# Kernel tuning notes

Measured on AMD Instinct MI355X. Metric: run time of the kernel, lower is better.

## Reference

```python
import jax, jax.numpy as jnp
import numpy as np

D = 128          # embed_dim
NSYM = 100000    # num_symbols
PAD = NSYM       # padding idx (zero row)
B = 2048         # query batch
FEW = 5          # support set size
M = 128          # max neighbors
KTAB = 64        # knn table width
K = 32           # knn_k topk
STEPS = 4        # process_steps
DM = 2 * D       # d_model for encoders (256)
HID = 2 * DM     # LSTM hidden (512)


def _cos(a, b):
    # torch F.cosine_similarity, eps=1e-8; a [B,1,d], b [B,N,d] -> [B,N]
    num = jnp.sum(a * b, axis=-1)
    den = jnp.maximum(jnp.linalg.norm(a, axis=-1) * jnp.linalg.norm(b, axis=-1), 1e-8)
    return num / den


def _l2n(x):
    return x / jnp.maximum(jnp.linalg.norm(x, axis=-1, keepdims=True), 1e-12)


def _neighbor_encoder(conn, ids, knn_tab, emb, gcn_w, gcn_w_b, gcn_b, gate_w, gate_b):
    rel = emb[conn[..., 0]]                      # [N,M,D]
    ent = emb[conn[..., 1]]                      # [N,M,D]
    center = emb[ids][:, None, :]                # [N,1,D]
    sim = _cos(center, ent)                      # [N,M]
    _, idx = jax.lax.top_k(sim, K)               # [N,K]
    rel_k = jnp.take_along_axis(rel, idx[..., None], axis=1)
    ent_k = jnp.take_along_axis(ent, idx[..., None], axis=1)
    h = jnp.concatenate([rel_k, ent_k], axis=-1) @ gcn_w.T + gcn_w_b + gcn_b
    struct = jnp.tanh(h.mean(axis=1))            # [N,D]
    # knn branch: gather knn neighbor ids, cosine topk, pad-relation embeds (zero row)
    kent = emb[knn_tab[ids]]                     # [N,KTAB,D]
    sim2 = _cos(center, kent)
    _, idx2 = jax.lax.top_k(sim2, K)
    kent_k = jnp.take_along_axis(kent, idx2[..., None], axis=1)
    pad_row = jax.lax.stop_gradient(emb[PAD])    # padding_idx row (zeros, no grad)
    krel = jnp.broadcast_to(pad_row, kent_k.shape)
    h2 = jnp.concatenate([krel, kent_k], axis=-1) @ gcn_w.T + gcn_w_b + gcn_b
    knn_mean = jnp.tanh(h2.mean(axis=1))         # [N,D]
    alpha = jax.nn.sigmoid(jnp.concatenate([struct, knn_mean], axis=-1) @ gate_w.T + gate_b)
    return (1.0 - alpha) * struct + alpha * knn_mean


def _support_encoder(x, p1_w, p1_b, p2_w, p2_b, ln_g, ln_b):
    o = jax.nn.relu(x @ p1_w.T + p1_b) @ p2_w.T + p2_b
    z = o + x
    mu = z.mean(axis=-1, keepdims=True)
    sig = z.std(axis=-1, ddof=1, keepdims=True)  # torch unbiased std
    return (z - mu) / (sig + 1e-3) * ln_g + ln_b


def _query_encoder(support, query, w_ih, w_hh, b_ih, b_hh):
    # attLSTM processing block; support [1,DM], query [B,DM]
    n = query.shape[0]
    h_r = jnp.zeros((n, HID), query.dtype)
    c = jnp.zeros((n, HID), query.dtype)
    h = query
    for _ in range(STEPS):
        g = query @ w_ih.T + b_ih + h_r @ w_hh.T + b_hh
        i, f, gg, o = jnp.split(g, 4, axis=-1)
        c = jax.nn.sigmoid(f) * c + jax.nn.sigmoid(i) * jnp.tanh(gg)
        h_ = jax.nn.sigmoid(o) * jnp.tanh(c)
        h = query + h_[:, :DM]
        attn = jax.nn.softmax(h @ support.T, axis=1)  # [B,1]
        r = attn @ support                             # [B,DM]
        h_r = jnp.concatenate([h, r], axis=1)
    return h


def _forward(query, support, q_l_conn, q_r_conn, s_l_conn, s_r_conn, knn_neighbors,
             emb, gcn_w, gcn_w_b, gcn_b, gate_w, gate_b,
             p1_w, p1_b, p2_w, p2_b, ln_g, ln_b, w_ih, w_hh, b_ih, b_hh):
    ne = lambda conn, ids: _neighbor_encoder(conn, ids, knn_neighbors, emb,
                                             gcn_w, gcn_w_b, gcn_b, gate_w, gate_b)
    ql = ne(q_l_conn, query[:, 0])
    qr = ne(q_r_conn, query[:, 1])
    sl = ne(s_l_conn, support[:, 0])
    sr = ne(s_r_conn, support[:, 1])
    qn = jnp.concatenate([ql, qr], axis=-1)   # [B,DM]
    sn = jnp.concatenate([sl, sr], axis=-1)   # [FEW,DM]
    se = lambda x: _support_encoder(x, p1_w, p1_b, p2_w, p2_b, ln_g, ln_b)
    support_g = se(sn).mean(axis=0, keepdims=True)  # [1,DM]
    query_g = se(qn)                                 # [B,DM]
    query_f = _l2n(_query_encoder(support_g, query_g, w_ih, w_hh, b_ih, b_hh))
    sg = _l2n(support_g[0])
    return query_f @ sg                              # [B]


def setup_inputs() -> dict:
    key = jax.random.key(0)
    ks = jax.random.split(key, 24)
    f = lambda i, shape, s=0.05: jax.random.normal(ks[i], shape, dtype=jnp.float32) * s
    ri = lambda i, shape: jax.random.randint(ks[i], shape, 0, NSYM).astype(jnp.int32)
    emb = f(0, (NSYM + 1, D), 0.5).at[PAD].set(0.0)
    return dict(
        query=ri(1, (B, 2)), support=ri(2, (FEW, 2)),
        q_l_conn=ri(3, (B, M, 2)),
        q_l_deg=jax.random.randint(ks[4], (B,), 1, M).astype(jnp.int32),
        q_r_conn=ri(5, (B, M, 2)),
        q_r_deg=jax.random.randint(ks[6], (B,), 1, M).astype(jnp.int32),
        s_l_conn=ri(7, (FEW, M, 2)),
        s_l_deg=jax.random.randint(ks[8], (FEW,), 1, M).astype(jnp.int32),
        s_r_conn=ri(9, (FEW, M, 2)),
        s_r_deg=jax.random.randint(ks[10], (FEW,), 1, M).astype(jnp.int32),
        knn_neighbors=ri(11, (NSYM + 1, KTAB)),
        emb=emb,
        gcn_w=f(12, (D, 2 * D)), gcn_w_b=f(13, (D,)),
        gcn_b=jnp.zeros((D,), jnp.float32),
        gate_w=f(14, (1, 2 * D)), gate_b=jnp.zeros((1,), jnp.float32),
        p1_w=f(15, (2 * DM, DM)), p1_b=f(16, (2 * DM,)),
        p2_w=f(17, (DM, 2 * DM)), p2_b=f(18, (DM,)),
        ln_g=jnp.ones((DM,), jnp.float32), ln_b=jnp.zeros((DM,), jnp.float32),
        w_ih=f(19, (4 * HID, DM)), w_hh=f(20, (4 * HID, HID)),
        b_ih=f(21, (4 * HID,)), b_hh=f(22, (4 * HID,)),
    )


def reference(query, support, q_l_conn, q_l_deg, q_r_conn, q_r_deg,
              s_l_conn, s_l_deg, s_r_conn, s_r_deg, knn_neighbors,
              emb, gcn_w, gcn_w_b, gcn_b, gate_w, gate_b,
              p1_w, p1_b, p2_w, p2_b, ln_g, ln_b, w_ih, w_hh, b_ih, b_hh):
    # degrees are computed-but-unused in this fork's neighbor_encoder (plain mean)
    return _forward(query, support, q_l_conn, q_r_conn, s_l_conn, s_r_conn, knn_neighbors,
                    emb, gcn_w, gcn_w_b, gcn_b, gate_w, gate_b,
                    p1_w, p1_b, p2_w, p2_b, ln_g, ln_b, w_ih, w_hh, b_ih, b_hh)
```

## Files before the change

### kernel.cpp

```cpp
#include <hip/hip_runtime.h>
#include <hip/hip_bf16.h>

typedef unsigned short u16;
typedef unsigned int u32;

constexpr int ED   = 128;
constexpr int MC   = 128;
constexpr int KT   = 64;
constexpr int KS   = 32;
constexpr int NB   = 2048;
constexpr int NF   = 5;
constexpr int DMM  = 256;
constexpr int NG   = 1024;
constexpr int PADID = 100000;
constexpr int NROWS = 2*NB + 2*NF;
constexpr int MT   = (NROWS + 63)/64;
constexpr int MP   = MT*64;

typedef __attribute__((ext_vector_type(8))) short short8;
typedef __attribute__((ext_vector_type(4))) float floatx4;

__device__ __forceinline__ float bf2f(u16 u){
  union { u32 i; float f; } v; v.i = ((u32)u) << 16; return v.f;
}
__device__ __forceinline__ float lo2f(u32 w){
  union { u32 i; float f; } v; v.i = w << 16; return v.f;
}
__device__ __forceinline__ float hi2f(u32 w){
  union { u32 i; float f; } v; v.i = w & 0xffff0000u; return v.f;
}
__device__ __forceinline__ u16 f2bf(float f){
  union { float f; u32 i; } v; v.f = f;
  u32 r = v.i + 0x7FFFu + ((v.i >> 16) & 1u);
  return (u16)(r >> 16);
}
__device__ __forceinline__ float sigf(float x){ return 1.f / (1.f + expf(-x)); }

__device__ __forceinline__ bool sniff(const void* ln_g){
  return *(const u32*)ln_g == 0x3F803F80u;
}

__device__ __forceinline__ float gld(const void* p, size_t i, bool bf){
  return bf ? bf2f(((const u16*)p)[i]) : ((const float*)p)[i];
}
__device__ __forceinline__ void ld4(const void* p, size_t i0, bool bf, float* o){
  if (bf){ uint2 w = *(const uint2*)((const u16*)p + i0);
           o[0]=lo2f(w.x); o[1]=hi2f(w.x); o[2]=lo2f(w.y); o[3]=hi2f(w.y); }
  else   { float4 v = *(const float4*)((const float*)p + i0);
           o[0]=v.x; o[1]=v.y; o[2]=v.z; o[3]=v.w; }
}
__device__ __forceinline__ void ld8(const void* p, size_t i0, bool bf, float* o){
  if (bf){
    uint4 v = *(const uint4*)((const u16*)p + i0);
    o[0]=lo2f(v.x); o[1]=hi2f(v.x); o[2]=lo2f(v.y); o[3]=hi2f(v.y);
    o[4]=lo2f(v.z); o[5]=hi2f(v.z); o[6]=lo2f(v.w); o[7]=hi2f(v.w);
  } else {
    const float* f = (const float*)p + i0;
    float4 a = *(const float4*)f, b = *(const float4*)(f + 4);
    o[0]=a.x; o[1]=a.y; o[2]=a.z; o[3]=a.w; o[4]=b.x; o[5]=b.y; o[6]=b.z; o[7]=b.w;
  }
}
__device__ __forceinline__ float dotw(const void* w, size_t i0, const float* x, int n, bool bf){
  float acc = 0.f, t[8];
  #pragma unroll 4
  for (int j = 0; j < n; j += 8){
    ld8(w, i0 + j, bf, t);
    #pragma unroll
    for (int q = 0; q < 8; q++) acc += t[q]*x[j+q];
  }
  return acc;
}

__device__ __forceinline__ float waveSum(float v){
  #pragma unroll
  for (int o = 32; o > 0; o >>= 1) v += __shfl_xor(v, o, 64);
  return v;
}
__device__ __forceinline__ float blockSum(float v, float* s8){
  int lane = threadIdx.x & 63, wid = threadIdx.x >> 6;
  v = waveSum(v);
  __syncthreads();
  if (lane == 0) s8[wid] = v;
  __syncthreads();
  return s8[0] + s8[1] + s8[2] + s8[3];
}
__device__ __forceinline__ float2 blockSum2(float a, float b, float* s8){
  int lane = threadIdx.x & 63, wid = threadIdx.x >> 6;
  a = waveSum(a); b = waveSum(b);
  __syncthreads();
  if (lane == 0){ s8[wid] = a; s8[4 + wid] = b; }
  __syncthreads();
  float2 r;
  r.x = s8[0] + s8[1] + s8[2] + s8[3];
  r.y = s8[4] + s8[5] + s8[6] + s8[7];
  return r;
}

__global__ __launch_bounds__(256) void neighbor_kernel(
    const int* __restrict__ query, const int* __restrict__ support,
    const int* __restrict__ qlc, const int* __restrict__ qrc,
    const int* __restrict__ slc, const int* __restrict__ srcc,
    const int* __restrict__ knnt, const void* __restrict__ emb,
    float* __restrict__ gA, float* __restrict__ gK, const void* __restrict__ ln_g)
{
  const bool bf = sniff(ln_g);
  int blk = blockIdx.x;
  const int* conn; int id;
  if (blk < NB)            { id = query[2*blk];                 conn = qlc + (size_t)blk*MC*2; }
  else if (blk < 2*NB)     { int r = blk - NB;   id = query[2*r+1];   conn = qrc + (size_t)r*MC*2; }
  else if (blk < 2*NB+NF)  { int r = blk - 2*NB; id = support[2*r];   conn = slc + (size_t)r*MC*2; }
  else                     { int r = blk - 2*NB - NF; id = support[2*r+1]; conn = srcc + (size_t)r*MC*2; }

  __shared__ float s_center[ED];
  __shared__ float s_sim[MC + KT];
  __shared__ float s_red[8];
  __shared__ int s_eid[MC + KT];
  __shared__ int s_selE[KS], s_selR[KS], s_selK[KS];
  __shared__ float s_mt[3][8][ED];

  const int tid = threadIdx.x, lane = tid & 63, wid = tid >> 6;

  if (tid < ED) s_center[tid] = gld(emb, (size_t)id*ED + tid, bf);
  if (tid < MC)           s_eid[tid] = conn[2*tid + 1];
  else if (tid < MC + KT) s_eid[tid] = knnt[(size_t)id*KT + (tid - MC)];

  float cpart = 0.f;
  if (tid < ED){ float c = s_center[tid]; cpart = c*c; }
  float cnorm = sqrtf(blockSum(cpart, s_red));

  const int g = lane & 15;
  float creg[8];
  #pragma unroll
  for (int j = 0; j < 8; j++) creg[j] = s_center[g*8 + j];

  #pragma unroll 4
  for (int m0 = wid*4; m0 < MC + KT; m0 += 16){
    int m = m0 + (lane >> 4);
    int eid = s_eid[m];
    float e[8];
    ld8(emb, (size_t)eid*ED + g*8, bf, e);
    float d = 0.f, q = 0.f;
    #pragma unroll
    for (int j = 0; j < 8; j++){ d += creg[j]*e[j]; q += e[j]*e[j]; }
    #pragma unroll
    for (int o = 8; o > 0; o >>= 1){ d += __shfl_xor(d, o, 64); q += __shfl_xor(q, o, 64); }
    if (g == 0) s_sim[m] = d / fmaxf(cnorm * sqrtf(q), 1e-8f);
  }
  __syncthreads();

  if (tid < MC){
    float v = s_sim[tid];
    int cnt = 0;
    #pragma unroll 8
    for (int j = 0; j < MC; j++){
      float w = s_sim[j];
      cnt += (w > v || (w == v && j < tid)) ? 1 : 0;
    }
    if (cnt < KS){ s_selR[cnt] = conn[2*tid]; s_selE[cnt] = s_eid[tid]; }
  } else if (tid < MC + KT){
    int t = tid - MC;
    float v = s_sim[MC + t];
    int cnt = 0;
    #pragma unroll 8
    for (int j = 0; j < KT; j++){
      float w = s_sim[MC + j];
      cnt += (w > v || (w == v && j < t)) ? 1 : 0;
    }
    if (cnt < KS) s_selK[cnt] = s_eid[MC + t];
  }
  __syncthreads();

  {
    const int slot = tid >> 5, c4 = (tid & 31)*4;
    float aR[4] = {0,0,0,0}, aE[4] = {0,0,0,0}, aK[4] = {0,0,0,0};
    #pragma unroll
    for (int k = 0; k < 4; k++){
      float t[4];
      ld4(emb, (size_t)s_selR[k*8 + slot]*ED + c4, bf, t);
      aR[0]+=t[0]; aR[1]+=t[1]; aR[2]+=t[2]; aR[3]+=t[3];
      ld4(emb, (size_t)s_selE[k*8 + slot]*ED + c4, bf, t);
      aE[0]+=t[0]; aE[1]+=t[1]; aE[2]+=t[2]; aE[3]+=t[3];
      ld4(emb, (size_t)s_selK[k*8 + slot]*ED + c4, bf, t);
      aK[0]+=t[0]; aK[1]+=t[1]; aK[2]+=t[2]; aK[3]+=t[3];
    }
    *(float4*)&s_mt[0][slot][c4] = make_float4(aR[0], aR[1], aR[2], aR[3]);
    *(float4*)&s_mt[1][slot][c4] = make_float4(aE[0], aE[1], aE[2], aE[3]);
    *(float4*)&s_mt[2][slot][c4] = make_float4(aK[0], aK[1], aK[2], aK[3]);
  }
  __syncthreads();
  {
    int dd = tid & (ED - 1), which = tid >> 7;
    float s = 0.f;
    #pragma unroll
    for (int p = 0; p < 8; p++) s += s_mt[which][p][dd];
    gA[(size_t)blk*DMM + which*ED + dd] = s * (1.f/KS);
    if (tid < ED){
      float sk = 0.f;
      #pragma unroll
      for (int p = 0; p < 8; p++) sk += s_mt[2][p][dd];
      gK[(size_t)blk*ED + dd] = sk * (1.f/KS);
    }
  }
}

__global__ __launch_bounds__(256) void gcn_gemm(
    const float* __restrict__ ARE, const float* __restrict__ AK,
    const void* __restrict__ gcn_w, const void* __restrict__ gcn_w_b,
    const void* __restrict__ gcn_b, float* __restrict__ C, const void* __restrict__ ln_g)
{
  const bool bf = sniff(ln_g);
  __shared__ float As2[16][68];
  __shared__ float Ws2[16][68];
  int tid = threadIdx.x;
  int n0 = blockIdx.x * 64;
  int mt = blockIdx.y;
  const float* A; int lda, K, woff; size_t cbase; int mtt;
  if (mt < MT){ A = ARE; lda = DMM; K = DMM; woff = 0;  cbase = 0;              mtt = mt; }
  else        { A = AK;  lda = ED;  K = ED;  woff = ED; cbase = (size_t)MP*ED;  mtt = mt - MT; }
  int m0 = mtt*64;

  int tx = tid & 15, ty = tid >> 4;
  int sn_ = tid & 63, kq = tid >> 6;
  size_t wbase = (size_t)(n0 + sn_)*DMM + woff;
  int ar = tid >> 2, ac = (tid & 3)*4;
  const float* ap = A + (size_t)(m0 + ar)*lda + ac;

  float acc[4][4];
  #pragma unroll
  for (int i = 0; i < 4; i++)
    #pragma unroll
    for (int j = 0; j < 4; j++) acc[i][j] = 0.f;

  for (int kc = 0; kc < K; kc += 16){
    __syncthreads();
    float4 av = *(const float4*)(ap + kc);
    As2[ac+0][ar] = av.x; As2[ac+1][ar] = av.y; As2[ac+2][ar] = av.z; As2[ac+3][ar] = av.w;
    float wt[4];
    ld4(gcn_w, wbase + kc + kq*4, bf, wt);
    Ws2[kq*4+0][sn_] = wt[0]; Ws2[kq*4+1][sn_] = wt[1];
    Ws2[kq*4+2][sn_] = wt[2]; Ws2[kq*4+3][sn_] = wt[3];
    __syncthreads();
    #pragma unroll
    for (int k = 0; k < 16; k++){
      float4 a = *(const float4*)&As2[k][ty*4];
      float4 b = *(const float4*)&Ws2[k][tx*4];
      acc[0][0] += a.x*b.x; acc[0][1] += a.x*b.y; acc[0][2] += a.x*b.z; acc[0][3] += a.x*b.w;
      acc[1][0] += a.y*b.x; acc[1][1] += a.y*b.y; acc[1][2] += a.y*b.z; acc[1][3] += a.y*b.w;
      acc[2][0] += a.z*b.x; acc[2][1] += a.z*b.y; acc[2][2] += a.z*b.z; acc[2][3] += a.z*b.w;
      acc[3][0] += a.w*b.x; acc[3][1] += a.w*b.y; acc[3][2] += a.w*b.z; acc[3][3] += a.w*b.w;
    }
  }

  float b4[4];
  #pragma unroll
  for (int j = 0; j < 4; j++){
    int n = n0 + tx*4 + j;
    b4[j] = gld(gcn_w_b, n, bf) + gld(gcn_b, n, bf);
  }
  #pragma unroll
  for (int i = 0; i < 4; i++){
    int row = m0 + ty*4 + i;
    float4 v = make_float4(acc[i][0]+b4[0], acc[i][1]+b4[1], acc[i][2]+b4[2], acc[i][3]+b4[3]);
    *(float4*)(C + cbase + (size_t)row*ED + n0 + tx*4) = v;
  }
}

__global__ __launch_bounds__(256) void mlp_enc_kernel(
    const float* __restrict__ gC, const void* __restrict__ gate_w,
    const void* __restrict__ gate_b,
    const void* __restrict__ p1_w, const void* __restrict__ p1_b,
    const void* __restrict__ p2_w, const void* __restrict__ p2_b,
    const void* __restrict__ ln_g, const void* __restrict__ ln_b,
    float* __restrict__ dst, int nrows)
{
  const bool bf = sniff(ln_g);
  constexpr int RPB = 8;
  __shared__ float x[RPB][DMM];
  __shared__ float hid[RPB][2*DMM];
  __shared__ float s_red[8];
  int tid = threadIdx.x;
  int r0 = blockIdx.x * RPB;

  {
    int rr = tid >> 5, c4 = (tid & 31) * 4;
    int row = r0 + rr;
    bool valid = row < nrows;
    int rowc = valid ? row : 0;
    int pairL, pairR;
    if (rowc < NB){ pairL = rowc;               pairR = NB + rowc; }
    else          { pairL = 2*NB + (rowc - NB); pairR = 2*NB + NF + (rowc - NB); }
    float4 pl1 = *(const float4*)(gC + (size_t)pairL*ED + c4);
    float4 pl2 = *(const float4*)(gC + (size_t)(MP + pairL)*ED + c4);
    float4 pr1 = *(const float4*)(gC + (size_t)pairR*ED + c4);
    float4 pr2 = *(const float4*)(gC + (size_t)(MP + pairR)*ED + c4);
    float sl[4] = {tanhf(pl1.x), tanhf(pl1.y), tanhf(pl1.z), tanhf(pl1.w)};
    float kl[4] = {tanhf(pl2.x), tanhf(pl2.y), tanhf(pl2.z), tanhf(pl2.w)};
    float sr[4] = {tanhf(pr1.x), tanhf(pr1.y), tanhf(pr1.z), tanhf(pr1.w)};
    float kr[4] = {tanhf(pr2.x), tanhf(pr2.y), tanhf(pr2.z), tanhf(pr2.w)};
    float gwS[4], gwK[4];
    ld4(gate_w, c4, bf, gwS);
    ld4(gate_w, ED + c4, bf, gwK);
    float gvL = 0.f, gvR = 0.f;
    #pragma unroll
    for (int i = 0; i < 4; i++){
      gvL += gwS[i]*sl[i] + gwK[i]*kl[i];
      gvR += gwS[i]*sr[i] + gwK[i]*kr[i];
    }
    #pragma unroll
    for (int o = 16; o > 0; o >>= 1){
      gvL += __shfl_xor(gvL, o, 64);
      gvR += __shfl_xor(gvR, o, 64);
    }
    float gb0 = gld(gate_b, 0, bf);
    float aL = sigf(gvL + gb0), aR = sigf(gvR + gb0);
    float4 xL, xR;
    xL.x = valid ? (1.f-aL)*sl[0] + aL*kl[0] : 0.f;
    xL.y = valid ? (1.f-aL)*sl[1] + aL*kl[1] : 0.f;
    xL.z = valid ? (1.f-aL)*sl[2] + aL*kl[2] : 0.f;
    xL.w = valid ? (1.f-aL)*sl[3] + aL*kl[3] : 0.f;
    xR.x = valid ? (1.f-aR)*sr[0] + aR*kr[0] : 0.f;
    xR.y = valid ? (1.f-aR)*sr[1] + aR*kr[1] : 0.f;
    xR.z = valid ? (1.f-aR)*sr[2] + aR*kr[2] : 0.f;
    xR.w = valid ? (1.f-aR)*sr[3] + aR*kr[3] : 0.f;
    *(float4*)&x[rr][c4]      = xL;
    *(float4*)&x[rr][ED + c4] = xR;
  }
  __syncthreads();

  {
    float acc0[RPB], acc1[RPB];
    #pragma unroll
    for (int r = 0; r < RPB; r++){ acc0[r] = 0.f; acc1[r] = 0.f; }
    for (int j8 = 0; j8 < DMM/8; j8++){
      float wa[8], wb[8];
      ld8(p1_w, (size_t)tid*DMM + j8*8, bf, wa);
      ld8(p1_w, (size_t)(tid+256)*DMM + j8*8, bf, wb);
      #pragma unroll
      for (int r = 0; r < RPB; r++){
        const float* xr = &x[r][j8*8];
        float s0 = 0.f, s1 = 0.f;
        #pragma unroll
        for (int q = 0; q < 8; q++){ float xv = xr[q]; s0 += wa[q]*xv; s1 += wb[q]*xv; }
        acc0[r] += s0; acc1[r] += s1;
      }
    }
    float bb0 = gld(p1_b, tid, bf), bb1 = gld(p1_b, tid + 256, bf);
    #pragma unroll
    for (int r = 0; r < RPB; r++){
      hid[r][tid]     = fmaxf(acc0[r] + bb0, 0.f);
      hid[r][tid+256] = fmaxf(acc1[r] + bb1, 0.f);
    }
  }
  __syncthreads();

  float zr[RPB];
  {
    #pragma unroll
    for (int r = 0; r < RPB; r++) zr[r] = 0.f;
    for (int j8 = 0; j8 < (2*DMM)/8; j8++){
      float wa[8];
      ld8(p2_w, (size_t)tid*(2*DMM) + j8*8, bf, wa);
      #pragma unroll
      for (int r = 0; r < RPB; r++){
        const float* hr = &hid[r][j8*8];
        float s0 = 0.f;
        #pragma unroll
        for (int q = 0; q < 8; q++) s0 += wa[q]*hr[q];
        zr[r] += s0;
      }
    }
    float bb = gld(p2_b, tid, bf);
    #pragma unroll
    for (int r = 0; r < RPB; r++) zr[r] += bb + x[r][tid];
  }

  float lg = gld(ln_g, tid, bf), lb = gld(ln_b, tid, bf);
  for (int r = 0; r < RPB; r++){
    float2 st = blockSum2(zr[r], zr[r]*zr[r], s_red);
    float mu = st.x * (1.f/DMM);
    float var = (st.y - (float)DMM*mu*mu) * (1.f/(DMM - 1));
    float sig = sqrtf(fmaxf(var, 0.f));
    if (r0 + r < nrows)
      dst[(size_t)(r0 + r)*DMM + tid] = (zr[r] - mu)/(sig + 1e-3f)*lg + lb;
  }
}

__global__ __launch_bounds__(256) void svec_kernel(
    const void* __restrict__ w_hh, const void* __restrict__ b_ih, const void* __restrict__ b_hh,
    const float* __restrict__ seS, float* __restrict__ cvec0, float* __restrict__ svec,
    float* __restrict__ sgn, const void* __restrict__ ln_g)
{
  const bool bf = sniff(ln_g);
  __shared__ float sg[DMM];
  __shared__ float s_red[8];
  int tid = threadIdx.x;
  float a = 0.f;
  for (int r = 0; r < NF; r++) a += seS[r*DMM + tid];
  a *= (1.f/NF);
  sg[tid] = a;
  __syncthreads();
  if (blockIdx.x == 0){
    float nn = blockSum(a*a, s_red);
    sgn[tid] = a / fmaxf(sqrtf(nn), 1e-12f);
  }
  int u = blockIdx.x * 256 + tid;
  int wrow = (u >> 8)*512 + (u & 255);
  cvec0[u] = gld(b_ih, wrow, bf) + gld(b_hh, wrow, bf);
  svec[u] = dotw(w_hh, (size_t)wrow*(2*DMM) + DMM, sg, DMM, bf);
}

__global__ __launch_bounds__(256) void gemm_gates(
    const float* __restrict__ A,
    const void* __restrict__ W, int wstride,
    const float* __restrict__ addvec, const float* __restrict__ addmat,
    float* __restrict__ C, const void* __restrict__ ln_g)
{
  const bool bf = sniff(ln_g);
  int tid = threadIdx.x;
  int n0 = blockIdx.x * 64, m0 = blockIdx.y * 64;

  if (bf){
    constexpr int KP = 136;
    __shared__ u16 As[64 * KP];
    __shared__ u16 Ws[64 * KP];
    const int wv = tid >> 6, lane = tid & 63;
    const int quad = lane >> 4, l16 = lane & 15;
    const int sr = tid >> 5, sc = tid & 31;

    floatx4 acc[4];
    #pragma unroll
    for (int t = 0; t < 4; t++) acc[t] = (floatx4){0.f, 0.f, 0.f, 0.f};

    for (int kc = 0; kc < 256; kc += 128){
      __syncthreads();
      #pragma unroll
      for (int i = 0; i < 8; i++){
        int r = i*8 + sr;
        float4 v = *(const float4*)(A + (size_t)(m0 + r)*256 + kc + sc*4);
        u32 p0 = (u32)f2bf(v.x) | ((u32)f2bf(v.y) << 16);
        u32 p1 = (u32)f2bf(v.z) | ((u32)f2bf(v.w) << 16);
        *(uint2*)&As[r*KP + sc*4] = make_uint2(p0, p1);
      }
      #pragma unroll
      for (int i = 0; i < 8; i++){
        int nn = i*8 + sr;
        int gn = n0 + nn;
        int wrow = (gn >> 8)*512 + (gn & 255);
        uint2 wv2 = *(const uint2*)((const u16*)W + (size_t)wrow*wstride + kc + sc*4);
        *(uint2*)&Ws[nn*KP + sc*4] = wv2;
      }
      __syncthreads();
      int am = wv*16 + l16;
      #pragma unroll
      for (int k1 = 0; k1 < 128; k1 += 32){
        int ko = k1 + quad*8;
        short8 af = *(const short8*)&As[am*KP + ko];
        #pragma unroll
        for (int t = 0; t < 4; t++){
          short8 bfr = *(const short8*)&Ws[(t*16 + l16)*KP + ko];
          acc[t] = __builtin_amdgcn_mfma_f32_16x16x32_bf16(af, bfr, acc[t], 0, 0, 0);
        }
      }
    }

    #pragma unroll
    for (int t = 0; t < 4; t++){
      int col = n0 + t*16 + l16;
      float av = addvec ? addvec[col] : 0.f;
      #pragma unroll
      for (int r = 0; r < 4; r++){
        int row = m0 + wv*16 + quad*4 + r;
        float val = acc[t][r] + av;
        if (addmat) val += addmat[(size_t)row*NG + col];
        C[(size_t)row*NG + col] = val;
      }
    }
    return;
  }

  {
    __shared__ float As2[16][68];
    __shared__ float Ws2[16][68];
    int tx = tid & 15, ty = tid >> 4;
    int sn_ = tid & 63, kq = tid >> 6;
    int gn = n0 + sn_;
    size_t wbase = (size_t)((gn >> 8)*512 + (gn & 255)) * wstride;
    int ar = tid >> 2, ac = (tid & 3) * 4;
    const float* ap = A + (size_t)(m0 + ar)*256 + ac;

    float acc[4][4];
    #pragma unroll
    for (int i = 0; i < 4; i++)
      #pragma unroll
      for (int j = 0; j < 4; j++) acc[i][j] = 0.f;

    for (int kc = 0; kc < 256; kc += 16){
      __syncthreads();
      float4 av = *(const float4*)(ap + kc);
      As2[ac+0][ar] = av.x; As2[ac+1][ar] = av.y; As2[ac+2][ar] = av.z; As2[ac+3][ar] = av.w;
      float wt[4];
      ld4(W, wbase + kc + kq*4, false, wt);
      Ws2[kq*4+0][sn_] = wt[0]; Ws2[kq*4+1][sn_] = wt[1];
      Ws2[kq*4+2][sn_] = wt[2]; Ws2[kq*4+3][sn_] = wt[3];
      __syncthreads();
      #pragma unroll
      for (int k = 0; k < 16; k++){
        float4 a = *(const float4*)&As2[k][ty*4];
        float4 b = *(const float4*)&Ws2[k][tx*4];
        acc[0][0] += a.x*b.x; acc[0][1] += a.x*b.y; acc[0][2] += a.x*b.z; acc[0][3] += a.x*b.w;
        acc[1][0] += a.y*b.x; acc[1][1] += a.y*b.y; acc[1][2] += a.y*b.z; acc[1][3] += a.y*b.w;
        acc[2][0] += a.z*b.x; acc[2][1] += a.z*b.y; acc[2][2] += a.z*b.z; acc[2][3] += a.z*b.w;
        acc[3][0] += a.w*b.x; acc[3][1] += a.w*b.y; acc[3][2] += a.w*b.z; acc[3][3] += a.w*b.w;
      }
    }

    float4 addc = make_float4(0.f, 0.f, 0.f, 0.f);
    if (addvec){
      float4 t = *(const float4*)(addvec + n0 + tx*4);
      addc.x = t.x; addc.y = t.y; addc.z = t.z; addc.w = t.w;
    }
    #pragma unroll
    for (int i = 0; i < 4; i++){
      int row = m0 + ty*4 + i;
      float4 v = make_float4(acc[i][0]+addc.x, acc[i][1]+addc.y, acc[i][2]+addc.z, acc[i][3]+addc.w);
      if (addmat){
        float4 t = *(const float4*)(addmat + (size_t)row*NG + n0 + tx*4);
        v.x += t.x; v.y += t.y; v.z += t.z; v.w += t.w;
      }
      *(float4*)(C + (size_t)row*NG + n0 + tx*4) = v;
    }
  }
}

__global__ __launch_bounds__(256) void lstm_elem(
    const float* __restrict__ g, const float* __restrict__ query_g,
    float* __restrict__ c, float* __restrict__ h, int first,
    const float* __restrict__ sgn, void* __restrict__ out, const void* __restrict__ ln_g)
{
  __shared__ float s_red[8];
  int b = blockIdx.x, j = threadIdx.x;
  const float* gb = g + (size_t)b*NG;
  float iv = gb[j], fv = gb[256 + j], gv = gb[512 + j], ov = gb[768 + j];
  float cc = first ? 0.f : c[(size_t)b*DMM + j];
  cc = sigf(fv)*cc + sigf(iv)*tanhf(gv);
  c[(size_t)b*DMM + j] = cc;
  float hh = query_g[(size_t)b*DMM + j] + sigf(ov)*tanhf(cc);
  h[(size_t)b*DMM + j] = hh;
  if (out){
    float2 st = blockSum2(hh*sgn[j], hh*hh, s_red);
    if (j == 0){
      float v = st.x / fmaxf(sqrtf(st.y), 1e-12f);
      if (sniff(ln_g)) ((__hip_bfloat16*)out)[b] = __float2bfloat16(v);
      else             ((float*)out)[b] = v;
    }
  }
}

extern "C" void kernel_launch(void* const* d_in, const int* in_sizes, int n_in,
                              void* d_out, int out_size, void* d_ws, size_t ws_size,
                              hipStream_t stream)
{
  const int* query   = (const int*)d_in[0];
  const int* support = (const int*)d_in[1];
  const int* qlc     = (const int*)d_in[2];
  const int* qrc     = (const int*)d_in[4];
  const int* slc     = (const int*)d_in[6];
  const int* srcc    = (const int*)d_in[8];
  const int* knnt    = (const int*)d_in[10];
  const void* emb     = d_in[11];
  const void* gcn_w   = d_in[12];
  const void* gcn_w_b = d_in[13];
  const void* gcn_b   = d_in[14];
  const void* gate_w  = d_in[15];
  const void* gate_b  = d_in[16];
  const void* p1_w    = d_in[17];
  const void* p1_b    = d_in[18];
  const void* p2_w    = d_in[19];
  const void* p2_b    = d_in[20];
  const void* ln_g    = d_in[21];
  const void* ln_b    = d_in[22];
  const void* w_ih    = d_in[23];
  const void* w_hh    = d_in[24];
  const void* b_ih    = d_in[25];
  const void* b_hh    = d_in[26];

  float* ws = (float*)d_ws + 64;
  size_t off = 0;
  float* query_g = ws + off; off += (size_t)NB*DMM;
  float* seS     = ws + off; off += NF*DMM;
  float* sgn     = ws + off; off += DMM;
  float* cvec0   = ws + off; off += NG;
  float* svec    = ws + off; off += NG;
  float* qx      = ws + off; off += (size_t)NB*NG;
  float* gbuf    = ws + off; off += (size_t)NB*NG;
  float* hbuf    = ws + off; off += (size_t)NB*DMM;
  float* cbuf    = ws + off; off += (size_t)NB*DMM;
  float* gA      = ws + off; off += (size_t)MP*DMM;
  float* gK      = ws + off; off += (size_t)MP*ED;
  float* gC      = ws + off; off += (size_t)2*MP*ED;

  neighbor_kernel<<<NROWS, 256, 0, stream>>>(
      query, support, qlc, qrc, slc, srcc, knnt, emb, gA, gK, ln_g);

  gcn_gemm<<<dim3(2, 2*MT), 256, 0, stream>>>(gA, gK, gcn_w, gcn_w_b, gcn_b, gC, ln_g);

  mlp_enc_kernel<<<(NB + NF + 7)/8, 256, 0, stream>>>(
      gC, gate_w, gate_b, p1_w, p1_b, p2_w, p2_b, ln_g, ln_b, query_g, NB + NF);

  svec_kernel<<<NG/256, 256, 0, stream>>>(w_hh, b_ih, b_hh, seS, cvec0, svec, sgn, ln_g);

  gemm_gates<<<dim3(NG/64, NB/64), 256, 0, stream>>>(query_g, w_ih, 256, cvec0, nullptr, qx, ln_g);

  lstm_elem<<<NB, 256, 0, stream>>>(qx, query_g, cbuf, hbuf, 1, nullptr, nullptr, ln_g);
  for (int s = 1; s < 4; s++){
    gemm_gates<<<dim3(NG/64, NB/64), 256, 0, stream>>>(hbuf, w_hh, 512, svec, qx, gbuf, ln_g);
    lstm_elem<<<NB, 256, 0, stream>>>(gbuf, query_g, cbuf, hbuf, 0,
                                      sgn, (s == 3) ? d_out : nullptr, ln_g);
  }

  (void)in_sizes; (void)n_in; (void)out_size; (void)ws_size;
}
```

Measured before the change: 431.6 us.

## Pre-transpose LSTM weights and use shuffle reduction in neighbor kernel

```diff
diff --git a/kernel.cpp b/kernel.cpp
--- a/kernel.cpp
+++ b/kernel.cpp
@@ -116,7 +116,6 @@
   __shared__ float s_red[8];
   __shared__ int s_eid[MC + KT];
   __shared__ int s_selE[KS], s_selR[KS], s_selK[KS];
-  __shared__ float s_mt[3][8][ED];
 
   const int tid = threadIdx.x, lane = tid & 63, wid = tid >> 6;
 
@@ -171,7 +170,8 @@
   __syncthreads();
 
   {
-    const int slot = tid >> 5, c4 = (tid & 31)*4;
+    const int slot = tid & 7;
+    const int c4 = (tid >> 3) * 4;
     float aR[4] = {0,0,0,0}, aE[4] = {0,0,0,0}, aK[4] = {0,0,0,0};
     #pragma unroll
     for (int k = 0; k < 4; k++){
@@ -183,22 +183,23 @@
       ld4(emb, (size_t)s_selK[k*8 + slot]*ED + c4, bf, t);
       aK[0]+=t[0]; aK[1]+=t[1]; aK[2]+=t[2]; aK[3]+=t[3];
     }
-    *(float4*)&s_mt[0][slot][c4] = make_float4(aR[0], aR[1], aR[2], aR[3]);
-    *(float4*)&s_mt[1][slot][c4] = make_float4(aE[0], aE[1], aE[2], aE[3]);
-    *(float4*)&s_mt[2][slot][c4] = make_float4(aK[0], aK[1], aK[2], aK[3]);
-  }
-  __syncthreads();
-  {
-    int dd = tid & (ED - 1), which = tid >> 7;
-    float s = 0.f;
-    #pragma unroll
-    for (int p = 0; p < 8; p++) s += s_mt[which][p][dd];
-    gA[(size_t)blk*DMM + which*ED + dd] = s * (1.f/KS);
-    if (tid < ED){
-      float sk = 0.f;
-      #pragma unroll
-      for (int p = 0; p < 8; p++) sk += s_mt[2][p][dd];
-      gK[(size_t)blk*ED + dd] = sk * (1.f/KS);
+    #pragma unroll
+    for (int off = 1; off < 8; off <<= 1){
+      #pragma unroll
+      for (int i = 0; i < 4; i++){
+        aR[i] += __shfl_xor(aR[i], off, 64);
+        aE[i] += __shfl_xor(aE[i], off, 64);
+        aK[i] += __shfl_xor(aK[i], off, 64);
+      }
+    }
+    if (slot == 0){
+      constexpr float s = 1.f/KS;
+      *(float4*)&gA[(size_t)blk*DMM + c4] =
+          make_float4(aR[0]*s, aR[1]*s, aR[2]*s, aR[3]*s);
+      *(float4*)&gA[(size_t)blk*DMM + ED + c4] =
+          make_float4(aE[0]*s, aE[1]*s, aE[2]*s, aE[3]*s);
+      *(float4*)&gK[(size_t)blk*ED + c4] =
+          make_float4(aK[0]*s, aK[1]*s, aK[2]*s, aK[3]*s);
     }
   }
 }
@@ -385,33 +386,81 @@
   }
 }
 
-__global__ __launch_bounds__(256) void svec_kernel(
-    const void* __restrict__ w_hh, const void* __restrict__ b_ih, const void* __restrict__ b_hh,
-    const float* __restrict__ seS, float* __restrict__ cvec0, float* __restrict__ svec,
+__global__ __launch_bounds__(256) void prep_kernel(
+    const void* __restrict__ w_ih, const void* __restrict__ w_hh,
+    const void* __restrict__ b_ih, const void* __restrict__ b_hh,
+    const float* __restrict__ seS,
+    float* __restrict__ WT_ih, float* __restrict__ WT_hh,
+    float* __restrict__ svec, float* __restrict__ cvec0,
     float* __restrict__ sgn, const void* __restrict__ ln_g)
 {
   const bool bf = sniff(ln_g);
-  __shared__ float sg[DMM];
-  __shared__ float s_red[8];
-  int tid = threadIdx.x;
-  float a = 0.f;
-  for (int r = 0; r < NF; r++) a += seS[r*DMM + tid];
-  a *= (1.f/NF);
-  sg[tid] = a;
-  __syncthreads();
-  if (blockIdx.x == 0){
-    float nn = blockSum(a*a, s_red);
-    sgn[tid] = a / fmaxf(sqrtf(nn), 1e-12f);
-  }
-  int u = blockIdx.x * 256 + tid;
-  int wrow = (u >> 8)*512 + (u & 255);
-  cvec0[u] = gld(b_ih, wrow, bf) + gld(b_hh, wrow, bf);
-  svec[u] = dotw(w_hh, (size_t)wrow*(2*DMM) + DMM, sg, DMM, bf);
+  const int b = blockIdx.x, tid = threadIdx.x;
+  if (b < 32){
+    const void* W = (b < 16) ? w_ih : w_hh;
+    const int wstride = (b < 16) ? 256 : 512;
+    float* WT = (b < 16) ? WT_ih : WT_hh;
+    const int n0 = (b & 15) * 64;
+    __shared__ float tile[64][65];
+    const int nl = tid >> 2, kq = tid & 3;
+    const int kl = tid >> 2, nq = tid & 3;
+    const int wrow = ((n0 + nl) >> 8)*512 + ((n0 + nl) & 255);
+    for (int kc = 0; kc < 256; kc += 64){
+      __syncthreads();
+      float t[16];
+      ld8(W, (size_t)wrow*wstride + kc + kq*16,     bf, t);
+      ld8(W, (size_t)wrow*wstride + kc + kq*16 + 8, bf, t + 8);
+      #pragma unroll
+      for (int i = 0; i < 16; i++) tile[nl][kq*16 + i] = t[i];
+      __syncthreads();
+      float o[16];
+      #pragma unroll
+      for (int i = 0; i < 16; i++) o[i] = tile[nq*16 + i][kl];
+      #pragma unroll
+      for (int i = 0; i < 16; i += 4)
+        *(float4*)&WT[(size_t)(kc + kl)*NG + n0 + nq*16 + i] =
+            make_float4(o[i], o[i+1], o[i+2], o[i+3]);
+    }
+  } else {
+    const int n0 = (b - 32) * 64;
+    __shared__ float sg[DMM];
+    __shared__ float part[64][4];
+    __shared__ float s_red[8];
+    if (tid < DMM){
+      float a = 0.f;
+      #pragma unroll
+      for (int r = 0; r < NF; r++) a += seS[r*DMM + tid];
+      sg[tid] = a * (1.f/NF);
+    }
+    __syncthreads();
+    if (b == 32){
+      float sq = (tid < DMM) ? sg[tid]*sg[tid] : 0.f;
+      float nn = blockSum(sq, s_red);
+      if (tid < DMM) sgn[tid] = sg[tid] / fmaxf(sqrtf(nn), 1e-12f);
+    }
+    const int nl = tid >> 2, q = tid & 3;
+    const int n = n0 + nl;
+    const int wrow = (n >> 8)*512 + (n & 255);
+    float acc = 0.f, t[8];
+    #pragma unroll
+    for (int k8 = 0; k8 < 8; k8++){
+      ld8(w_hh, (size_t)wrow*(2*DMM) + DMM + q*64 + k8*8, bf, t);
+      #pragma unroll
+      for (int j = 0; j < 8; j++) acc += t[j]*sg[q*64 + k8*8 + j];
+    }
+    part[nl][q] = acc;
+    __syncthreads();
+    if (tid < 64){
+      svec[n0 + tid] = part[tid][0] + part[tid][1] + part[tid][2] + part[tid][3];
+      const int wr2 = ((n0 + tid) >> 8)*512 + ((n0 + tid) & 255);
+      cvec0[n0 + tid] = gld(b_ih, wr2, bf) + gld(b_hh, wr2, bf);
+    }
+  }
 }
 
 __global__ __launch_bounds__(256) void gemm_gates(
     const float* __restrict__ A,
-    const void* __restrict__ W, int wstride,
+    const void* __restrict__ W, const float* __restrict__ WT, int wstride,
     const float* __restrict__ addvec, const float* __restrict__ addmat,
     float* __restrict__ C, const void* __restrict__ ln_g)
 {
@@ -479,14 +528,13 @@
   }
 
   {
-    __shared__ float As2[16][68];
-    __shared__ float Ws2[16][68];
+    __shared__ float As2[32][68];
+    __shared__ float Ws2[32][68];
     int tx = tid & 15, ty = tid >> 4;
-    int sn_ = tid & 63, kq = tid >> 6;
-    int gn = n0 + sn_;
-    size_t wbase = (size_t)((gn >> 8)*512 + (gn & 255)) * wstride;
-    int ar = tid >> 2, ac = (tid & 3) * 4;
-    const float* ap = A + (size_t)(m0 + ar)*256 + ac;
+    int arow = tid >> 2, acol = (tid & 3) * 8;
+    int wkr = tid >> 3, wnc = (tid & 7) * 8;
+    const float* ap = A + (size_t)(m0 + arow)*256 + acol;
+    const float* wp = WT + (size_t)wkr*NG + n0 + wnc;
 
     float acc[4][4];
     #pragma unroll
@@ -494,17 +542,21 @@
       #pragma unroll
       for (int j = 0; j < 4; j++) acc[i][j] = 0.f;
 
-    for (int kc = 0; kc < 256; kc += 16){
+    for (int kc = 0; kc < 256; kc += 32){
       __syncthreads();
-      float4 av = *(const float4*)(ap + kc);
-      As2[ac+0][ar] = av.x; As2[ac+1][ar] = av.y; As2[ac+2][ar] = av.z; As2[ac+3][ar] = av.w;
-      float wt[4];
-      ld4(W, wbase + kc + kq*4, false, wt);
-      Ws2[kq*4+0][sn_] = wt[0]; Ws2[kq*4+1][sn_] = wt[1];
-      Ws2[kq*4+2][sn_] = wt[2]; Ws2[kq*4+3][sn_] = wt[3];
+      float4 a0 = *(const float4*)(ap + kc);
+      float4 a1 = *(const float4*)(ap + kc + 4);
+      As2[acol+0][arow] = a0.x; As2[acol+1][arow] = a0.y;
+      As2[acol+2][arow] = a0.z; As2[acol+3][arow] = a0.w;
+      As2[acol+4][arow] = a1.x; As2[acol+5][arow] = a1.y;
+      As2[acol+6][arow] = a1.z; As2[acol+7][arow] = a1.w;
+      float4 w0 = *(const float4*)(wp + (size_t)kc*NG);
+      float4 w1 = *(const float4*)(wp + (size_t)kc*NG + 4);
+      *(float4*)&Ws2[wkr][wnc]     = w0;
+      *(float4*)&Ws2[wkr][wnc + 4] = w1;
       __syncthreads();
       #pragma unroll
-      for (int k = 0; k < 16; k++){
+      for (int k = 0; k < 32; k++){
         float4 a = *(const float4*)&As2[k][ty*4];
         float4 b = *(const float4*)&Ws2[k][tx*4];
         acc[0][0] += a.x*b.x; acc[0][1] += a.x*b.y; acc[0][2] += a.x*b.z; acc[0][3] += a.x*b.w;
@@ -595,6 +647,8 @@
   float* gbuf    = ws + off; off += (size_t)NB*NG;
   float* hbuf    = ws + off; off += (size_t)NB*DMM;
   float* cbuf    = ws + off; off += (size_t)NB*DMM;
+  float* WT_ih   = ws + off; off += (size_t)DMM*NG;
+  float* WT_hh   = ws + off; off += (size_t)DMM*NG;
   float* gA      = ws + off; off += (size_t)MP*DMM;
   float* gK      = ws + off; off += (size_t)MP*ED;
   float* gC      = ws + off; off += (size_t)2*MP*ED;
@@ -607,13 +661,16 @@
   mlp_enc_kernel<<<(NB + NF + 7)/8, 256, 0, stream>>>(
       gC, gate_w, gate_b, p1_w, p1_b, p2_w, p2_b, ln_g, ln_b, query_g, NB + NF);
 
-  svec_kernel<<<NG/256, 256, 0, stream>>>(w_hh, b_ih, b_hh, seS, cvec0, svec, sgn, ln_g);
-
-  gemm_gates<<<dim3(NG/64, NB/64), 256, 0, stream>>>(query_g, w_ih, 256, cvec0, nullptr, qx, ln_g);
+  prep_kernel<<<48, 256, 0, stream>>>(
+      w_ih, w_hh, b_ih, b_hh, seS, WT_ih, WT_hh, svec, cvec0, sgn, ln_g);
+
+  gemm_gates<<<dim3(NG/64, NB/64), 256, 0, stream>>>(
+      query_g, w_ih, WT_ih, 256, cvec0, nullptr, qx, ln_g);
 
   lstm_elem<<<NB, 256, 0, stream>>>(qx, query_g, cbuf, hbuf, 1, nullptr, nullptr, ln_g);
   for (int s = 1; s < 4; s++){
-    gemm_gates<<<dim3(NG/64, NB/64), 256, 0, stream>>>(hbuf, w_hh, 512, svec, qx, gbuf, ln_g);
+    gemm_gates<<<dim3(NG/64, NB/64), 256, 0, stream>>>(
+        hbuf, w_hh, WT_hh, 512, svec, qx, gbuf, ln_g);
     lstm_elem<<<NB, 256, 0, stream>>>(gbuf, query_g, cbuf, hbuf, 0,
                                       sgn, (s == 3) ? d_out : nullptr, ln_g);
   }
```

New measurement: 433.7 us. About the same (+0.5%).
